# Kernel optimization log

Measured on AMD Instinct MI355X. Metric: run time of the kernel, lower is better.

Reference implementation:

```python
import jax, jax.numpy as jnp
import numpy as np

N = 100000
E = 1250000
D = 64
R = 16


def _glorot(key, shape):
    fan_in, fan_out = shape[-2], shape[-1]
    lim = jnp.sqrt(6.0 / (fan_in + fan_out))
    return jax.random.uniform(key, shape, jnp.float32, -lim, lim)


def setup_inputs() -> dict:
    key = jax.random.key(0)
    ks = jax.random.split(key, 9)
    x = jax.random.normal(ks[0], (N, D), jnp.float32)
    edge_index = jax.random.randint(ks[1], (2, E), 0, N, jnp.int64 if jax.config.jax_enable_x64 else jnp.int32).astype(jnp.int32)
    edge_type = jax.random.randint(ks[2], (E,), 0, R).astype(jnp.int32)
    return {
        "x": x,
        "edge_index": edge_index,
        "edge_type": edge_type,
        "W1": _glorot(ks[3], (R, D, D)),
        "sw1": _glorot(ks[4], (D, D)),
        "b1": jnp.zeros((D,), jnp.float32),
        "W2": _glorot(ks[5], (R, D, D)),
        "sw2": _glorot(ks[6], (D, D)),
        "b2": jnp.zeros((D,), jnp.float32),
    }


def _rgcn_layer(x, src, dst, edge_type, W, sw, b, residual):
    # self transform [N, O]
    out = x @ sw
    # per-relation transform of all nodes: [N, R, O] (avoids [E, D, O] gathered weights,
    # same math as bmm(x_j, W[edge_type]))
    xW = jnp.einsum('nd,rdo->nro', x, W)
    msg = xW[src, edge_type]                      # [E, O] per-edge messages
    agg = jax.ops.segment_sum(msg, dst, num_segments=N)  # scatter-add aggregate
    out = out + agg
    if residual:
        out = out + x  # Identity residual (in == out channels)
    out = out + b
    return jax.nn.relu(out)


def reference(x, edge_index, edge_type, W1, sw1, b1, W2, sw2, b2):
    src, dst = edge_index[0], edge_index[1]
    # layer 1: residual=True; layer 2: encoding=False -> no residual.
    # activation (relu) applied after every layer by RGCN.forward; dropout p=0 / eval -> no-op.
    h = _rgcn_layer(x, src, dst, edge_type, W1, sw1, b1, residual=True)
    h = _rgcn_layer(h, src, dst, edge_type, W2, sw2, b2, residual=False)
    return h
```

## Files before the change

kernel.cpp:

```cpp
#include <hip/hip_runtime.h>
#include <hip/hip_bf16.h>

#define NN 100000
#define NE 1250000
#define DD 64
#define RR 16
#define NP 17
#define NTILE 6250

typedef __attribute__((ext_vector_type(8))) short s16x8;
typedef __attribute__((ext_vector_type(4))) float f32x4;

static __device__ __forceinline__ unsigned short f2bf(float v) {
    __hip_bfloat16 h = __float2bfloat16(v);
    return __builtin_bit_cast(unsigned short, h);
}
static __device__ __forceinline__ float bf2f(unsigned short u) {
    unsigned int w = ((unsigned int)u) << 16;
    return __builtin_bit_cast(float, w);
}
static __device__ __forceinline__ unsigned int pack2(float a, float b) {
    return ((unsigned int)f2bf(b) << 16) | (unsigned int)f2bf(a);
}


__global__ void hist_dst(const int* __restrict__ dst, int* __restrict__ cnt) {
    int e = blockIdx.x * 256 + threadIdx.x;
    if (e < NE) atomicAdd(&cnt[dst[e]], 1);
}

__global__ __launch_bounds__(256) void scan1(const int* __restrict__ cnt,
                                             int* __restrict__ rp, int* __restrict__ part) {
    __shared__ int s[256];
    int i = blockIdx.x * 256 + threadIdx.x;
    int v = (i < NN) ? cnt[i] : 0;
    s[threadIdx.x] = v;
    __syncthreads();
    for (int off = 1; off < 256; off <<= 1) {
        int t = (threadIdx.x >= off) ? s[threadIdx.x - off] : 0;
        __syncthreads();
        s[threadIdx.x] += t;
        __syncthreads();
    }
    if (i < NN) rp[i] = s[threadIdx.x] - v;
    if (threadIdx.x == 255) part[blockIdx.x] = s[255];
}

#define NBLK_SCAN 391
__global__ void scan2(int* __restrict__ part, int* __restrict__ rp) {
    __shared__ int s[NBLK_SCAN];
    if (threadIdx.x < NBLK_SCAN) s[threadIdx.x] = part[threadIdx.x];
    __syncthreads();
    if (threadIdx.x == 0) {
        int acc = 0;
        for (int b = 0; b < NBLK_SCAN; ++b) { int t = s[b]; s[b] = acc; acc += t; }
        rp[NN] = NE;
    }
    __syncthreads();
    if (threadIdx.x < NBLK_SCAN) part[threadIdx.x] = s[threadIdx.x];
}

__global__ void scan3(int* __restrict__ rp, const int* __restrict__ part, int* __restrict__ cur) {
    int i = blockIdx.x * 256 + threadIdx.x;
    if (i < NN) {
        int v = rp[i] + part[blockIdx.x];
        rp[i] = v;
        cur[i] = v;
    }
}

__global__ void scatter_dst(const int* __restrict__ src, const int* __restrict__ dst,
                            const int* __restrict__ et, int* __restrict__ cur,
                            int* __restrict__ sg) {
    int e = blockIdx.x * 256 + threadIdx.x;
    if (e >= NE) return;
    int p = atomicAdd(&cur[dst[e]], 1);
    sg[p] = et[e] * NN + src[e];
}


__global__ void prep_w2(const float* __restrict__ W1, const float* __restrict__ sw1,
                        const float* __restrict__ W2, const float* __restrict__ sw2,
                        unsigned short* __restrict__ wt) {
    int i = blockIdx.x * 256 + threadIdx.x;
    if (i >= 2 * NP * DD * DD) return;
    int d = i & 63;
    int o = (i >> 6) & 63;
    int p = (i >> 12) % NP;
    int l = i / (NP * DD * DD);
    const float* src;
    if (p < 16) src = (l ? W2 : W1) + p * DD * DD;
    else        src = (l ? sw2 : sw1);
    wt[i] = f2bf(src[d * DD + o]);
}

__global__ void prep_x2(const float* __restrict__ x, unsigned short* __restrict__ xb) {
    int i = blockIdx.x * blockDim.x + threadIdx.x;
    if (i < NN * DD) xb[i] = f2bf(x[i]);
}

__global__ __launch_bounds__(256) void xw_kernel(
    const unsigned short* __restrict__ xb,
    const unsigned short* __restrict__ wt,
    unsigned short* __restrict__ tab)
{
    const int wid  = threadIdx.x >> 6;
    const int lane = threadIdx.x & 63;
    const int c = lane & 15;
    const int q = lane >> 4;
    const int t = blockIdx.x * 4 + wid;
    if (t >= NTILE) return;
    const int n0 = t * 16;
    const int p0 = blockIdx.y * 4;
    const int p1 = min(p0 + 4, NP);

    const unsigned short* xrow = xb + (size_t)(n0 + c) * DD + q * 8;
    s16x8 b0 = *(const s16x8*)(xrow);
    s16x8 b1 = *(const s16x8*)(xrow + 32);

    for (int p = p0; p < p1; ++p) {
        const unsigned short* wp = wt + p * (DD * DD);
        uint2* orow = (uint2*)(tab + ((size_t)p * NN + n0 + c) * DD);
        #pragma unroll
        for (int nb = 0; nb < 4; ++nb) {
            const unsigned short* wrow = wp + (nb * 16 + c) * DD + q * 8;
            s16x8 a0 = *(const s16x8*)(wrow);
            s16x8 a1 = *(const s16x8*)(wrow + 32);
            f32x4 acc = {0.f, 0.f, 0.f, 0.f};
            acc = __builtin_amdgcn_mfma_f32_16x16x32_bf16(a0, b0, acc, 0, 0, 0);
            acc = __builtin_amdgcn_mfma_f32_16x16x32_bf16(a1, b1, acc, 0, 0, 0);
            uint2 pk;
            pk.x = pack2(acc[0], acc[1]);
            pk.y = pack2(acc[2], acc[3]);
            orow[nb * 4 + q] = pk;
        }
    }
}

__global__ __launch_bounds__(256) void agg_kernel(
    const unsigned short* __restrict__ tab,
    const int* __restrict__ rp,
    const int* __restrict__ sg,
    const float* __restrict__ bias,
    const float* __restrict__ xres,
    float* __restrict__ outf,
    unsigned short* __restrict__ outb)
{
    const int wid  = threadIdx.x >> 6;
    const int lane = threadIdx.x & 63;
    const int n = blockIdx.x * 4 + wid;
    const int h  = lane >> 5;
    const int ol = lane & 31;

    float a0 = 0.f, a1 = 0.f;
    int e = rp[n];
    const int e1 = rp[n + 1];
    for (; e + 4 <= e1; e += 4) {
        int r0 = sg[e + h];
        int r1 = sg[e + 2 + h];
        unsigned int u0 = *(const unsigned int*)(tab + (size_t)r0 * DD + ol * 2);
        unsigned int u1 = *(const unsigned int*)(tab + (size_t)r1 * DD + ol * 2);
        a0 += bf2f((unsigned short)u0) + bf2f((unsigned short)u1);
        a1 += bf2f((unsigned short)(u0 >> 16)) + bf2f((unsigned short)(u1 >> 16));
    }
    for (; e + 2 <= e1; e += 2) {
        int r0 = sg[e + h];
        unsigned int u0 = *(const unsigned int*)(tab + (size_t)r0 * DD + ol * 2);
        a0 += bf2f((unsigned short)u0);
        a1 += bf2f((unsigned short)(u0 >> 16));
    }
    if (e < e1 && h == 0) {
        int r0 = sg[e];
        unsigned int u0 = *(const unsigned int*)(tab + (size_t)r0 * DD + ol * 2);
        a0 += bf2f((unsigned short)u0);
        a1 += bf2f((unsigned short)(u0 >> 16));
    }
    a0 += __shfl_xor(a0, 32, 64);
    a1 += __shfl_xor(a1, 32, 64);

    {
        unsigned int u = *(const unsigned int*)(tab + ((size_t)16 * NN + n) * DD + ol * 2);
        a0 += bf2f((unsigned short)u);
        a1 += bf2f((unsigned short)(u >> 16));
    }
    const float2 bv = *(const float2*)(bias + ol * 2);
    a0 += bv.x; a1 += bv.y;
    if (xres) {
        const float2 rv = *(const float2*)(xres + (size_t)n * DD + ol * 2);
        a0 += rv.x; a1 += rv.y;
    }
    a0 = fmaxf(a0, 0.f);
    a1 = fmaxf(a1, 0.f);

    if (h == 0) {
        if (outb)
            *(unsigned int*)(outb + (size_t)n * DD + ol * 2) = pack2(a0, a1);
        if (outf) {
            float2 v = {a0, a1};
            *(float2*)(outf + (size_t)n * DD + ol * 2) = v;
        }
    }
}


extern "C" void kernel_launch(void* const* d_in, const int* in_sizes, int n_in,
                              void* d_out, int out_size, void* d_ws, size_t ws_size,
                              hipStream_t stream)
{
    (void)in_sizes; (void)n_in; (void)out_size; (void)ws_size;
    const float* x    = (const float*)d_in[0];
    const int*   ei   = (const int*)d_in[1];
    const int*   et   = (const int*)d_in[2];
    const float* W1   = (const float*)d_in[3];
    const float* sw1  = (const float*)d_in[4];
    const float* b1   = (const float*)d_in[5];
    const float* W2   = (const float*)d_in[6];
    const float* sw2  = (const float*)d_in[7];
    const float* b2   = (const float*)d_in[8];
    float* out = (float*)d_out;

    const int* src = ei;
    const int* dst = ei + NE;

    char* ws = (char*)d_ws;

    unsigned short* tab  = (unsigned short*)(ws);
    unsigned short* xb   = (unsigned short*)(ws + 217600000);
    unsigned short* h1b  = (unsigned short*)(ws + 230400000);
    unsigned short* wt2  = (unsigned short*)(ws + 243200000);
    int* sg   = (int*)(ws + 243478528);
    int* rp   = (int*)(ws + 248478528);
    int* cur  = (int*)(ws + 248878544);
    int* cnt  = (int*)(ws + 249278544);
    int* part = (int*)(ws + 249678544);

    const int NB_E    = (NE + 255) / 256;
    const int NB_ELEM = (NN * DD + 255) / 256;

    hipMemsetAsync(cnt, 0, NN * sizeof(int), stream);
    hist_dst<<<NB_E, 256, 0, stream>>>(dst, cnt);
    scan1<<<NBLK_SCAN, 256, 0, stream>>>(cnt, rp, part);
    scan2<<<1, 512, 0, stream>>>(part, rp);
    scan3<<<NBLK_SCAN, 256, 0, stream>>>(rp, part, cur);
    scatter_dst<<<NB_E, 256, 0, stream>>>(src, dst, et, cur, sg);

    prep_w2<<<(2 * NP * DD * DD + 255) / 256, 256, 0, stream>>>(W1, sw1, W2, sw2, wt2);
    prep_x2<<<NB_ELEM, 256, 0, stream>>>(x, xb);

    const int NB_XW  = (NTILE + 3) / 4;
    const int NB_AGG = NN / 4;

    xw_kernel<<<dim3(NB_XW, 5), 256, 0, stream>>>(xb, wt2, tab);
    agg_kernel<<<NB_AGG, 256, 0, stream>>>(tab, rp, sg, b1, x, nullptr, h1b);

    xw_kernel<<<dim3(NB_XW, 5), 256, 0, stream>>>(h1b, wt2 + NP * DD * DD, tab);
    agg_kernel<<<NB_AGG, 256, 0, stream>>>(tab, rp, sg, b2, nullptr, out, nullptr);
}
```

Before: 598.2 us.

## Split relation table into two halves to shrink gather working set

Edges are now bucketed by destination and relation half (relations 0-7 and 8-15), and each layer computes and aggregates in two phases, each using a 9-slot (or 8-slot) transformed-feature table instead of a 17-slot one. A float carry buffer holds the partial sum between phases. The intent is to halve the footprint of the randomly gathered table so more of it stays in cache. The cost is extra launches, a carry write and read per node, and twice the passes over the CSR offsets.

```diff
diff --git a/kernel.cpp b/kernel.cpp
--- a/kernel.cpp
+++ b/kernel.cpp
@@ -5,8 +5,10 @@
 #define NE 1250000
 #define DD 64
 #define RR 16
-#define NP 17
+#define NSLOT 9
 #define NTILE 6250
+#define NBINS 200000
+#define NBLK2 782
 
 typedef __attribute__((ext_vector_type(8))) short s16x8;
 typedef __attribute__((ext_vector_type(4))) float f32x4;
@@ -24,16 +26,17 @@
 }
 
 
-__global__ void hist_dst(const int* __restrict__ dst, int* __restrict__ cnt) {
+__global__ void hist_key(const int* __restrict__ dst, const int* __restrict__ et,
+                         int* __restrict__ cnt) {
     int e = blockIdx.x * 256 + threadIdx.x;
-    if (e < NE) atomicAdd(&cnt[dst[e]], 1);
+    if (e < NE) atomicAdd(&cnt[dst[e] * 2 + (et[e] >> 3)], 1);
 }
 
 __global__ __launch_bounds__(256) void scan1(const int* __restrict__ cnt,
                                              int* __restrict__ rp, int* __restrict__ part) {
     __shared__ int s[256];
     int i = blockIdx.x * 256 + threadIdx.x;
-    int v = (i < NN) ? cnt[i] : 0;
+    int v = (i < NBINS) ? cnt[i] : 0;
     s[threadIdx.x] = v;
     __syncthreads();
     for (int off = 1; off < 256; off <<= 1) {
@@ -42,40 +45,40 @@
         s[threadIdx.x] += t;
         __syncthreads();
     }
-    if (i < NN) rp[i] = s[threadIdx.x] - v;
+    if (i < NBINS) rp[i] = s[threadIdx.x] - v;
     if (threadIdx.x == 255) part[blockIdx.x] = s[255];
 }
 
-#define NBLK_SCAN 391
-__global__ void scan2(int* __restrict__ part, int* __restrict__ rp) {
-    __shared__ int s[NBLK_SCAN];
-    if (threadIdx.x < NBLK_SCAN) s[threadIdx.x] = part[threadIdx.x];
+__global__ __launch_bounds__(1024) void scan2(int* __restrict__ part, int* __restrict__ rp) {
+    __shared__ int s[NBLK2];
+    if (threadIdx.x < NBLK2) s[threadIdx.x] = part[threadIdx.x];
     __syncthreads();
     if (threadIdx.x == 0) {
         int acc = 0;
-        for (int b = 0; b < NBLK_SCAN; ++b) { int t = s[b]; s[b] = acc; acc += t; }
-        rp[NN] = NE;
+        for (int b = 0; b < NBLK2; ++b) { int t = s[b]; s[b] = acc; acc += t; }
+        rp[NBINS] = NE;
     }
     __syncthreads();
-    if (threadIdx.x < NBLK_SCAN) part[threadIdx.x] = s[threadIdx.x];
+    if (threadIdx.x < NBLK2) part[threadIdx.x] = s[threadIdx.x];
 }
 
 __global__ void scan3(int* __restrict__ rp, const int* __restrict__ part, int* __restrict__ cur) {
     int i = blockIdx.x * 256 + threadIdx.x;
-    if (i < NN) {
+    if (i < NBINS) {
         int v = rp[i] + part[blockIdx.x];
         rp[i] = v;
         cur[i] = v;
     }
 }
 
-__global__ void scatter_dst(const int* __restrict__ src, const int* __restrict__ dst,
+__global__ void scatter_key(const int* __restrict__ src, const int* __restrict__ dst,
                             const int* __restrict__ et, int* __restrict__ cur,
                             int* __restrict__ sg) {
     int e = blockIdx.x * 256 + threadIdx.x;
     if (e >= NE) return;
-    int p = atomicAdd(&cur[dst[e]], 1);
-    sg[p] = et[e] * NN + src[e];
+    int r = et[e];
+    int p = atomicAdd(&cur[dst[e] * 2 + (r >> 3)], 1);
+    sg[p] = (r & 7) * NN + src[e];
 }
 
 
@@ -83,15 +86,18 @@
                         const float* __restrict__ W2, const float* __restrict__ sw2,
                         unsigned short* __restrict__ wt) {
     int i = blockIdx.x * 256 + threadIdx.x;
-    if (i >= 2 * NP * DD * DD) return;
+    if (i >= 2 * 17 * DD * DD) return;
     int d = i & 63;
     int o = (i >> 6) & 63;
-    int p = (i >> 12) % NP;
-    int l = i / (NP * DD * DD);
-    const float* src;
-    if (p < 16) src = (l ? W2 : W1) + p * DD * DD;
-    else        src = (l ? sw2 : sw1);
-    wt[i] = f2bf(src[d * DD + o]);
+    int s = (i >> 12) % 17;
+    int l = i / (17 * DD * DD);
+    const float* W  = l ? W2 : W1;
+    const float* sw = l ? sw2 : sw1;
+    const float* srcp;
+    if (s < 8)       srcp = W + s * DD * DD;
+    else if (s == 8) srcp = sw;
+    else             srcp = W + (s - 1) * DD * DD;
+    wt[i] = f2bf(srcp[d * DD + o]);
 }
 
 __global__ void prep_x2(const float* __restrict__ x, unsigned short* __restrict__ xb) {
@@ -102,7 +108,8 @@
 __global__ __launch_bounds__(256) void xw_kernel(
     const unsigned short* __restrict__ xb,
     const unsigned short* __restrict__ wt,
-    unsigned short* __restrict__ tab)
+    unsigned short* __restrict__ tab,
+    int np)
 {
     const int wid  = threadIdx.x >> 6;
     const int lane = threadIdx.x & 63;
@@ -111,8 +118,8 @@
     const int t = blockIdx.x * 4 + wid;
     if (t >= NTILE) return;
     const int n0 = t * 16;
-    const int p0 = blockIdx.y * 4;
-    const int p1 = min(p0 + 4, NP);
+    const int p0 = blockIdx.y * 3;
+    const int p1 = min(p0 + 3, np);
 
     const unsigned short* xrow = xb + (size_t)(n0 + c) * DD + q * 8;
     s16x8 b0 = *(const s16x8*)(xrow);
@@ -139,12 +146,14 @@
 
 __global__ __launch_bounds__(256) void agg_kernel(
     const unsigned short* __restrict__ tab,
-    const int* __restrict__ rp,
+    const int* __restrict__ rp2,
     const int* __restrict__ sg,
+    int phase,
     const float* __restrict__ bias,
     const float* __restrict__ xres,
-    float* __restrict__ outf,
-    unsigned short* __restrict__ outb)
+    float* __restrict__ carry,
+    unsigned short* __restrict__ outb,
+    float* __restrict__ outf)
 {
     const int wid  = threadIdx.x >> 6;
     const int lane = threadIdx.x & 63;
@@ -153,8 +162,8 @@
     const int ol = lane & 31;
 
     float a0 = 0.f, a1 = 0.f;
-    int e = rp[n];
-    const int e1 = rp[n + 1];
+    int e = rp2[n * 2 + phase];
+    const int e1 = rp2[n * 2 + phase + 1];
     for (; e + 4 <= e1; e += 4) {
         int r0 = sg[e + h];
         int r1 = sg[e + 2 + h];
@@ -178,26 +187,32 @@
     a0 += __shfl_xor(a0, 32, 64);
     a1 += __shfl_xor(a1, 32, 64);
 
-    {
-        unsigned int u = *(const unsigned int*)(tab + ((size_t)16 * NN + n) * DD + ol * 2);
+    if (phase == 0) {
+        unsigned int u = *(const unsigned int*)(tab + ((size_t)8 * NN + n) * DD + ol * 2);
         a0 += bf2f((unsigned short)u);
         a1 += bf2f((unsigned short)(u >> 16));
-    }
-    const float2 bv = *(const float2*)(bias + ol * 2);
-    a0 += bv.x; a1 += bv.y;
-    if (xres) {
-        const float2 rv = *(const float2*)(xres + (size_t)n * DD + ol * 2);
-        a0 += rv.x; a1 += rv.y;
-    }
-    a0 = fmaxf(a0, 0.f);
-    a1 = fmaxf(a1, 0.f);
-
-    if (h == 0) {
-        if (outb)
-            *(unsigned int*)(outb + (size_t)n * DD + ol * 2) = pack2(a0, a1);
-        if (outf) {
+        const float2 bv = *(const float2*)(bias + ol * 2);
+        a0 += bv.x; a1 += bv.y;
+        if (xres) {
+            const float2 rv = *(const float2*)(xres + (size_t)n * DD + ol * 2);
+            a0 += rv.x; a1 += rv.y;
+        }
+        if (h == 0) {
             float2 v = {a0, a1};
-            *(float2*)(outf + (size_t)n * DD + ol * 2) = v;
+            *(float2*)(carry + (size_t)n * DD + ol * 2) = v;
+        }
+    } else {
+        const float2 cv = *(const float2*)(carry + (size_t)n * DD + ol * 2);
+        a0 += cv.x; a1 += cv.y;
+        a0 = fmaxf(a0, 0.f);
+        a1 = fmaxf(a1, 0.f);
+        if (h == 0) {
+            if (outb)
+                *(unsigned int*)(outb + (size_t)n * DD + ol * 2) = pack2(a0, a1);
+            if (outf) {
+                float2 v = {a0, a1};
+                *(float2*)(outf + (size_t)n * DD + ol * 2) = v;
+            }
         }
     }
 }
@@ -224,35 +239,41 @@
 
     char* ws = (char*)d_ws;
 
-    unsigned short* tab  = (unsigned short*)(ws);
-    unsigned short* xb   = (unsigned short*)(ws + 217600000);
-    unsigned short* h1b  = (unsigned short*)(ws + 230400000);
-    unsigned short* wt2  = (unsigned short*)(ws + 243200000);
-    int* sg   = (int*)(ws + 243478528);
-    int* rp   = (int*)(ws + 248478528);
-    int* cur  = (int*)(ws + 248878544);
-    int* cnt  = (int*)(ws + 249278544);
-    int* part = (int*)(ws + 249678544);
+    unsigned short* tab   = (unsigned short*)(ws);
+    unsigned short* xb    = (unsigned short*)(ws + 115200000);
+    unsigned short* h1b   = (unsigned short*)(ws + 128000000);
+    float*          carry = (float*)(ws + 140800000);
+    unsigned short* wt2   = (unsigned short*)(ws + 166400000);
+    int* sg   = (int*)(ws + 166678528);
+    int* rp2  = (int*)(ws + 171678528);
+    int* cur  = (int*)(ws + 172478532);
+    int* cnt  = (int*)(ws + 173278532);
+    int* part = (int*)(ws + 174078532);
 
     const int NB_E    = (NE + 255) / 256;
     const int NB_ELEM = (NN * DD + 255) / 256;
 
-    hipMemsetAsync(cnt, 0, NN * sizeof(int), stream);
-    hist_dst<<<NB_E, 256, 0, stream>>>(dst, cnt);
-    scan1<<<NBLK_SCAN, 256, 0, stream>>>(cnt, rp, part);
-    scan2<<<1, 512, 0, stream>>>(part, rp);
-    scan3<<<NBLK_SCAN, 256, 0, stream>>>(rp, part, cur);
-    scatter_dst<<<NB_E, 256, 0, stream>>>(src, dst, et, cur, sg);
-
-    prep_w2<<<(2 * NP * DD * DD + 255) / 256, 256, 0, stream>>>(W1, sw1, W2, sw2, wt2);
+    hipMemsetAsync(cnt, 0, NBINS * sizeof(int), stream);
+    hist_key<<<NB_E, 256, 0, stream>>>(dst, et, cnt);
+    scan1<<<NBLK2, 256, 0, stream>>>(cnt, rp2, part);
+    scan2<<<1, 1024, 0, stream>>>(part, rp2);
+    scan3<<<NBLK2, 256, 0, stream>>>(rp2, part, cur);
+    scatter_key<<<NB_E, 256, 0, stream>>>(src, dst, et, cur, sg);
+
+    prep_w2<<<(2 * 17 * DD * DD + 255) / 256, 256, 0, stream>>>(W1, sw1, W2, sw2, wt2);
     prep_x2<<<NB_ELEM, 256, 0, stream>>>(x, xb);
 
     const int NB_XW  = (NTILE + 3) / 4;
     const int NB_AGG = NN / 4;
-
-    xw_kernel<<<dim3(NB_XW, 5), 256, 0, stream>>>(xb, wt2, tab);
-    agg_kernel<<<NB_AGG, 256, 0, stream>>>(tab, rp, sg, b1, x, nullptr, h1b);
-
-    xw_kernel<<<dim3(NB_XW, 5), 256, 0, stream>>>(h1b, wt2 + NP * DD * DD, tab);
-    agg_kernel<<<NB_AGG, 256, 0, stream>>>(tab, rp, sg, b2, nullptr, out, nullptr);
-}
+    const int WPL = 17 * DD * DD;
+
+    xw_kernel<<<dim3(NB_XW, 3), 256, 0, stream>>>(xb, wt2, tab, 9);
+    agg_kernel<<<NB_AGG, 256, 0, stream>>>(tab, rp2, sg, 0, b1, x, carry, nullptr, nullptr);
+    xw_kernel<<<dim3(NB_XW, 3), 256, 0, stream>>>(xb, wt2 + 9 * DD * DD, tab, 8);
+    agg_kernel<<<NB_AGG, 256, 0, stream>>>(tab, rp2, sg, 1, nullptr, nullptr, carry, h1b, nullptr);
+
+    xw_kernel<<<dim3(NB_XW, 3), 256, 0, stream>>>(h1b, wt2 + WPL, tab, 9);
+    agg_kernel<<<NB_AGG, 256, 0, stream>>>(tab, rp2, sg, 0, b2, nullptr, carry, nullptr, nullptr);
+    xw_kernel<<<dim3(NB_XW, 3), 256, 0, stream>>>(h1b, wt2 + WPL + 9 * DD * DD, tab, 8);
+    agg_kernel<<<NB_AGG, 256, 0, stream>>>(tab, rp2, sg, 1, nullptr, nullptr, carry, nullptr, out);
+}
```

Measured after the change: 675.6 us. 12.9% more time.

## Compute transforms only for used (relation, source) pairs and aggregate via edge chunks

Applied to the files above, without the earlier changes.

Builds a compacted list of the (relation, source) keys that actually appear in the edge list. The per-relation transform is computed only for those rows instead of for all 16 relations times every node, which shrinks the intermediate table that gets written and read. The self-transform, bias and residual move into separate fp32 kernels that write a carry buffer. Aggregation switches from one wave per destination node to fixed edge chunks, with segmented sums flushed by float atomics, and a finalize kernel applies ReLU. The cost is extra preprocessing passes (flag, scan, remap), more kernel launches, float atomic traffic, and non-deterministic summation order.

```diff
diff --git a/kernel.cpp b/kernel.cpp
--- a/kernel.cpp
+++ b/kernel.cpp
@@ -5,8 +5,10 @@
 #define NE 1250000
 #define DD 64
 #define RR 16
-#define NP 17
-#define NTILE 6250
+#define NKEY 1600000
+#define NTILEC 78125
+#define NBLK_SCAN 391
+#define NBLK_KEY 6250
 
 typedef __attribute__((ext_vector_type(8))) short s16x8;
 typedef __attribute__((ext_vector_type(4))) float f32x4;
@@ -24,6 +26,62 @@
 }
 
 
+__global__ void flag_key(const int* __restrict__ src, const int* __restrict__ et,
+                         unsigned char* __restrict__ flagK) {
+    int e = blockIdx.x * 256 + threadIdx.x;
+    if (e < NE) flagK[et[e] * NN + src[e]] = 1;
+}
+
+__global__ __launch_bounds__(256) void scanA(const unsigned char* __restrict__ flagK,
+                                             int* __restrict__ rowmap, int* __restrict__ partK) {
+    __shared__ int s[256];
+    int i = blockIdx.x * 256 + threadIdx.x;
+    int v = flagK[i] ? 1 : 0;
+    s[threadIdx.x] = v;
+    __syncthreads();
+    for (int off = 1; off < 256; off <<= 1) {
+        int t = (threadIdx.x >= off) ? s[threadIdx.x - off] : 0;
+        __syncthreads();
+        s[threadIdx.x] += t;
+        __syncthreads();
+    }
+    rowmap[i] = s[threadIdx.x] - v;
+    if (threadIdx.x == 255) partK[blockIdx.x] = s[255];
+}
+
+__global__ __launch_bounds__(1024) void scanB(int* __restrict__ partK) {
+    __shared__ int s[1024];
+    int t = threadIdx.x;
+    int b0 = t * 7, b1 = min(b0 + 7, NBLK_KEY);
+    int loc[7];
+    int sum = 0;
+    for (int j = b0; j < b1; ++j) { loc[j - b0] = partK[j]; sum += loc[j - b0]; }
+    s[t] = sum;
+    __syncthreads();
+    for (int off = 1; off < 1024; off <<= 1) {
+        int v = (t >= off) ? s[t - off] : 0;
+        __syncthreads();
+        s[t] += v;
+        __syncthreads();
+    }
+    int excl = s[t] - sum;
+    for (int j = b0; j < b1; ++j) { int v = loc[j - b0]; partK[j] = excl; excl += v; }
+}
+
+__global__ void scanC_emit(const unsigned char* __restrict__ flagK, int* __restrict__ rowmap,
+                           const int* __restrict__ partK,
+                           int* __restrict__ rsrc, int* __restrict__ rrel) {
+    int i = blockIdx.x * 256 + threadIdx.x;
+    int rid = rowmap[i] + partK[blockIdx.x];
+    rowmap[i] = rid;
+    if (flagK[i]) {
+        int rel = i / NN;
+        rsrc[rid] = i - rel * NN;
+        rrel[rid] = rel;
+    }
+}
+
+
 __global__ void hist_dst(const int* __restrict__ dst, int* __restrict__ cnt) {
     int e = blockIdx.x * 256 + threadIdx.x;
     if (e < NE) atomicAdd(&cnt[dst[e]], 1);
@@ -46,15 +104,13 @@
     if (threadIdx.x == 255) part[blockIdx.x] = s[255];
 }
 
-#define NBLK_SCAN 391
-__global__ void scan2(int* __restrict__ part, int* __restrict__ rp) {
+__global__ void scan2(int* __restrict__ part) {
     __shared__ int s[NBLK_SCAN];
     if (threadIdx.x < NBLK_SCAN) s[threadIdx.x] = part[threadIdx.x];
     __syncthreads();
     if (threadIdx.x == 0) {
         int acc = 0;
         for (int b = 0; b < NBLK_SCAN; ++b) { int t = s[b]; s[b] = acc; acc += t; }
-        rp[NN] = NE;
     }
     __syncthreads();
     if (threadIdx.x < NBLK_SCAN) part[threadIdx.x] = s[threadIdx.x];
@@ -69,29 +125,38 @@
     }
 }
 
-__global__ void scatter_dst(const int* __restrict__ src, const int* __restrict__ dst,
-                            const int* __restrict__ et, int* __restrict__ cur,
-                            int* __restrict__ sg) {
+__global__ void scatter2(const int* __restrict__ src, const int* __restrict__ dst,
+                         const int* __restrict__ et, const int* __restrict__ rowmap,
+                         int* __restrict__ cur, int2* __restrict__ sgd) {
     int e = blockIdx.x * 256 + threadIdx.x;
     if (e >= NE) return;
-    int p = atomicAdd(&cur[dst[e]], 1);
-    sg[p] = et[e] * NN + src[e];
-}
-
-
-__global__ void prep_w2(const float* __restrict__ W1, const float* __restrict__ sw1,
-                        const float* __restrict__ W2, const float* __restrict__ sw2,
-                        unsigned short* __restrict__ wt) {
-    int i = blockIdx.x * 256 + threadIdx.x;
-    if (i >= 2 * NP * DD * DD) return;
+    int d = dst[e];
+    int row = rowmap[et[e] * NN + src[e]];
+    int p = atomicAdd(&cur[d], 1);
+    sgd[p] = make_int2(row, d);
+}
+
+
+__global__ void prep_w(const float* __restrict__ W1, const float* __restrict__ W2,
+                       unsigned short* __restrict__ wt) {
+    int i = blockIdx.x * 256 + threadIdx.x;
+    if (i >= 2 * RR * DD * DD) return;
     int d = i & 63;
     int o = (i >> 6) & 63;
-    int p = (i >> 12) % NP;
-    int l = i / (NP * DD * DD);
-    const float* src;
-    if (p < 16) src = (l ? W2 : W1) + p * DD * DD;
-    else        src = (l ? sw2 : sw1);
-    wt[i] = f2bf(src[d * DD + o]);
+    int r = (i >> 12) & 15;
+    int l = i >> 16;
+    const float* W = l ? W2 : W1;
+    wt[i] = f2bf(W[(r * DD + d) * DD + o]);
+}
+
+__global__ void prep_swT(const float* __restrict__ sw1, const float* __restrict__ sw2,
+                         float* __restrict__ swT) {
+    int i = blockIdx.x * 256 + threadIdx.x;
+    if (i >= 2 * DD * DD) return;
+    int d = i & 63;
+    int o = (i >> 6) & 63;
+    int l = i >> 12;
+    swT[i] = (l ? sw2 : sw1)[d * DD + o];
 }
 
 __global__ void prep_x2(const float* __restrict__ x, unsigned short* __restrict__ xb) {
@@ -99,28 +164,37 @@
     if (i < NN * DD) xb[i] = f2bf(x[i]);
 }
 
-__global__ __launch_bounds__(256) void xw_kernel(
+
+__global__ __launch_bounds__(256) void xw_c(
     const unsigned short* __restrict__ xb,
     const unsigned short* __restrict__ wt,
-    unsigned short* __restrict__ tab)
+    const int* __restrict__ rsrc,
+    const int* __restrict__ rrel,
+    unsigned short* __restrict__ tabc)
 {
     const int wid  = threadIdx.x >> 6;
     const int lane = threadIdx.x & 63;
     const int c = lane & 15;
     const int q = lane >> 4;
-    const int t = blockIdx.x * 4 + wid;
-    if (t >= NTILE) return;
-    const int n0 = t * 16;
-    const int p0 = blockIdx.y * 4;
-    const int p1 = min(p0 + 4, NP);
-
-    const unsigned short* xrow = xb + (size_t)(n0 + c) * DD + q * 8;
+    const int tile = blockIdx.x * 4 + wid;
+    if (tile >= NTILEC) return;
+    const int row0 = tile * 16;
+
+    const int myrel = rrel[row0 + c];
+    const int r_lo = __shfl(myrel, 0, 64);
+    if (r_lo > 15) return;
+    const int r_hi = min(__shfl(myrel, 15, 64), 15);
+
+    const int srcn = rsrc[row0 + c];
+    const unsigned short* xrow = xb + (size_t)srcn * DD + q * 8;
     s16x8 b0 = *(const s16x8*)(xrow);
     s16x8 b1 = *(const s16x8*)(xrow + 32);
 
-    for (int p = p0; p < p1; ++p) {
-        const unsigned short* wp = wt + p * (DD * DD);
-        uint2* orow = (uint2*)(tab + ((size_t)p * NN + n0 + c) * DD);
+    uint2* orow = (uint2*)(tabc + (size_t)(row0 + c) * DD);
+
+    for (int r = r_lo; r <= r_hi; ++r) {
+        const unsigned short* wp = wt + r * (DD * DD);
+        const bool mine = (myrel == r);
         #pragma unroll
         for (int nb = 0; nb < 4; ++nb) {
             const unsigned short* wrow = wp + (nb * 16 + c) * DD + q * 8;
@@ -129,77 +203,112 @@
             f32x4 acc = {0.f, 0.f, 0.f, 0.f};
             acc = __builtin_amdgcn_mfma_f32_16x16x32_bf16(a0, b0, acc, 0, 0, 0);
             acc = __builtin_amdgcn_mfma_f32_16x16x32_bf16(a1, b1, acc, 0, 0, 0);
-            uint2 pk;
-            pk.x = pack2(acc[0], acc[1]);
-            pk.y = pack2(acc[2], acc[3]);
-            orow[nb * 4 + q] = pk;
+            if (mine) {
+                uint2 pk;
+                pk.x = pack2(acc[0], acc[1]);
+                pk.y = pack2(acc[2], acc[3]);
+                orow[nb * 4 + q] = pk;
+            }
         }
     }
 }
 
+__global__ __launch_bounds__(256) void self_f32(
+    const float* __restrict__ h, const float* __restrict__ swT,
+    const float* __restrict__ bias, const float* __restrict__ xres,
+    float* __restrict__ carry)
+{
+    int idx = blockIdx.x * 256 + threadIdx.x;
+    if (idx >= NN * DD) return;
+    int o = idx & 63;
+    int n = idx >> 6;
+    const float4* xrow = (const float4*)(h + (size_t)n * DD);
+    const float4* srow = (const float4*)(swT + o * DD);
+    float acc = bias[o];
+    if (xres) acc += xres[idx];
+    #pragma unroll
+    for (int j = 0; j < 16; ++j) {
+        float4 a = xrow[j], w = srow[j];
+        acc += a.x * w.x + a.y * w.y + a.z * w.z + a.w * w.w;
+    }
+    carry[idx] = acc;
+}
+
+__global__ __launch_bounds__(256) void self_bf(
+    const unsigned short* __restrict__ hb, const float* __restrict__ swT,
+    const float* __restrict__ bias, float* __restrict__ carry)
+{
+    int idx = blockIdx.x * 256 + threadIdx.x;
+    if (idx >= NN * DD) return;
+    int o = idx & 63;
+    int n = idx >> 6;
+    const unsigned int* hrow = (const unsigned int*)(hb + (size_t)n * DD);
+    const float2* srow = (const float2*)(swT + o * DD);
+    float acc = bias[o];
+    #pragma unroll
+    for (int j = 0; j < 32; ++j) {
+        unsigned int u = hrow[j];
+        float2 w = srow[j];
+        acc += bf2f((unsigned short)u) * w.x + bf2f((unsigned short)(u >> 16)) * w.y;
+    }
+    carry[idx] = acc;
+}
+
+#define CHUNK 64
 __global__ __launch_bounds__(256) void agg_kernel(
-    const unsigned short* __restrict__ tab,
-    const int* __restrict__ rp,
-    const int* __restrict__ sg,
-    const float* __restrict__ bias,
-    const float* __restrict__ xres,
-    float* __restrict__ outf,
-    unsigned short* __restrict__ outb)
+    const unsigned int* __restrict__ tab32,
+    const int2* __restrict__ sgd,
+    float* __restrict__ carry)
 {
     const int wid  = threadIdx.x >> 6;
     const int lane = threadIdx.x & 63;
-    const int n = blockIdx.x * 4 + wid;
     const int h  = lane >> 5;
     const int ol = lane & 31;
+    const int e0 = (blockIdx.x * 4 + wid) * CHUNK;
+    if (e0 >= NE) return;
 
     float a0 = 0.f, a1 = 0.f;
-    int e = rp[n];
-    const int e1 = rp[n + 1];
-    for (; e + 4 <= e1; e += 4) {
-        int r0 = sg[e + h];
-        int r1 = sg[e + 2 + h];
-        unsigned int u0 = *(const unsigned int*)(tab + (size_t)r0 * DD + ol * 2);
-        unsigned int u1 = *(const unsigned int*)(tab + (size_t)r1 * DD + ol * 2);
-        a0 += bf2f((unsigned short)u0) + bf2f((unsigned short)u1);
-        a1 += bf2f((unsigned short)(u0 >> 16)) + bf2f((unsigned short)(u1 >> 16));
-    }
-    for (; e + 2 <= e1; e += 2) {
-        int r0 = sg[e + h];
-        unsigned int u0 = *(const unsigned int*)(tab + (size_t)r0 * DD + ol * 2);
-        a0 += bf2f((unsigned short)u0);
-        a1 += bf2f((unsigned short)(u0 >> 16));
-    }
-    if (e < e1 && h == 0) {
-        int r0 = sg[e];
-        unsigned int u0 = *(const unsigned int*)(tab + (size_t)r0 * DD + ol * 2);
-        a0 += bf2f((unsigned short)u0);
-        a1 += bf2f((unsigned short)(u0 >> 16));
-    }
-    a0 += __shfl_xor(a0, 32, 64);
-    a1 += __shfl_xor(a1, 32, 64);
-
-    {
-        unsigned int u = *(const unsigned int*)(tab + ((size_t)16 * NN + n) * DD + ol * 2);
-        a0 += bf2f((unsigned short)u);
-        a1 += bf2f((unsigned short)(u >> 16));
-    }
-    const float2 bv = *(const float2*)(bias + ol * 2);
-    a0 += bv.x; a1 += bv.y;
-    if (xres) {
-        const float2 rv = *(const float2*)(xres + (size_t)n * DD + ol * 2);
-        a0 += rv.x; a1 += rv.y;
-    }
-    a0 = fmaxf(a0, 0.f);
-    a1 = fmaxf(a1, 0.f);
-
-    if (h == 0) {
-        if (outb)
-            *(unsigned int*)(outb + (size_t)n * DD + ol * 2) = pack2(a0, a1);
-        if (outf) {
-            float2 v = {a0, a1};
-            *(float2*)(outf + (size_t)n * DD + ol * 2) = v;
+    int cur = -1;
+    for (int base = 0; base < CHUNK; base += 16) {
+        int rowk[8], dk[8];
+        unsigned int uk[8];
+        #pragma unroll
+        for (int j = 0; j < 8; ++j) {
+            int e = e0 + base + 2 * j + h;
+            if (e < NE) { int2 g = sgd[e]; rowk[j] = g.x; dk[j] = g.y; }
+            else dk[j] = -1;
         }
-    }
+        #pragma unroll
+        for (int j = 0; j < 8; ++j)
+            if (dk[j] >= 0) uk[j] = tab32[(size_t)rowk[j] * 32 + ol];
+        #pragma unroll
+        for (int j = 0; j < 8; ++j) {
+            if (dk[j] < 0) continue;
+            if (dk[j] != cur) {
+                if (cur >= 0) {
+                    unsafeAtomicAdd(&carry[(size_t)cur * DD + ol * 2],     a0);
+                    unsafeAtomicAdd(&carry[(size_t)cur * DD + ol * 2 + 1], a1);
+                }
+                a0 = 0.f; a1 = 0.f;
+                cur = dk[j];
+            }
+            a0 += bf2f((unsigned short)uk[j]);
+            a1 += bf2f((unsigned short)(uk[j] >> 16));
+        }
+    }
+    if (cur >= 0) {
+        unsafeAtomicAdd(&carry[(size_t)cur * DD + ol * 2],     a0);
+        unsafeAtomicAdd(&carry[(size_t)cur * DD + ol * 2 + 1], a1);
+    }
+}
+
+__global__ void fin_kernel(const float* __restrict__ carry,
+                           unsigned short* __restrict__ outb, float* __restrict__ outf) {
+    int i = blockIdx.x * 256 + threadIdx.x;
+    if (i >= NN * DD) return;
+    float v = fmaxf(carry[i], 0.f);
+    if (outb) outb[i] = f2bf(v);
+    if (outf) outf[i] = v;
 }
 
 
@@ -219,40 +328,58 @@
     const float* b2   = (const float*)d_in[8];
     float* out = (float*)d_out;
 
-    const int* src = ei;
-    const int* dst = ei + NE;
+    const int* srcA = ei;
+    const int* dstA = ei + NE;
 
     char* ws = (char*)d_ws;
-
-    unsigned short* tab  = (unsigned short*)(ws);
-    unsigned short* xb   = (unsigned short*)(ws + 217600000);
-    unsigned short* h1b  = (unsigned short*)(ws + 230400000);
-    unsigned short* wt2  = (unsigned short*)(ws + 243200000);
-    int* sg   = (int*)(ws + 243478528);
-    int* rp   = (int*)(ws + 248478528);
-    int* cur  = (int*)(ws + 248878544);
-    int* cnt  = (int*)(ws + 249278544);
-    int* part = (int*)(ws + 249678544);
+    unsigned short* tabc  = (unsigned short*)(ws);
+    unsigned short* xb    = (unsigned short*)(ws + 160000000);
+    unsigned short* h1b   = (unsigned short*)(ws + 172800000);
+    float*          carry = (float*)(ws + 185600000);
+    unsigned short* wt2   = (unsigned short*)(ws + 211200000);
+    float*          swT   = (float*)(ws + 211462144);
+    int2*           sgd   = (int2*)(ws + 211494912);
+    int*            rowmap= (int*)(ws + 221494912);
+    unsigned char*  flagK = (unsigned char*)(ws + 227894912);
+    int*            rsrc  = (int*)(ws + 229494912);
+    int*            rrel  = (int*)(ws + 234499008);
+    int*            cnt   = (int*)(ws + 239503104);
+    int*            rp    = (int*)(ws + 239903104);
+    int*            cur   = (int*)(ws + 240303120);
+    int*            partD = (int*)(ws + 240703120);
+    int*            partK = (int*)(ws + 240704720);
 
     const int NB_E    = (NE + 255) / 256;
     const int NB_ELEM = (NN * DD + 255) / 256;
+    const int NB_XWC  = (NTILEC + 3) / 4;
+    const int NB_AGG  = (NE + 4 * CHUNK - 1) / (4 * CHUNK);
+
+    hipMemsetAsync(flagK, 0, 1600000, stream);
+    hipMemsetAsync(rsrc, 0, 5004096, stream);
+    hipMemsetAsync(rrel, 0x3f, 5004096, stream);
+    flag_key<<<NB_E, 256, 0, stream>>>(srcA, et, flagK);
+    scanA<<<NBLK_KEY, 256, 0, stream>>>(flagK, rowmap, partK);
+    scanB<<<1, 1024, 0, stream>>>(partK);
+    scanC_emit<<<NBLK_KEY, 256, 0, stream>>>(flagK, rowmap, partK, rsrc, rrel);
 
     hipMemsetAsync(cnt, 0, NN * sizeof(int), stream);
-    hist_dst<<<NB_E, 256, 0, stream>>>(dst, cnt);
-    scan1<<<NBLK_SCAN, 256, 0, stream>>>(cnt, rp, part);
-    scan2<<<1, 512, 0, stream>>>(part, rp);
-    scan3<<<NBLK_SCAN, 256, 0, stream>>>(rp, part, cur);
-    scatter_dst<<<NB_E, 256, 0, stream>>>(src, dst, et, cur, sg);
-
-    prep_w2<<<(2 * NP * DD * DD + 255) / 256, 256, 0, stream>>>(W1, sw1, W2, sw2, wt2);
+    hist_dst<<<NB_E, 256, 0, stream>>>(dstA, cnt);
+    scan1<<<NBLK_SCAN, 256, 0, stream>>>(cnt, rp, partD);
+    scan2<<<1, 512, 0, stream>>>(partD);
+    scan3<<<NBLK_SCAN, 256, 0, stream>>>(rp, partD, cur);
+    scatter2<<<NB_E, 256, 0, stream>>>(srcA, dstA, et, rowmap, cur, sgd);
+
+    prep_w<<<(2 * RR * DD * DD + 255) / 256, 256, 0, stream>>>(W1, W2, wt2);
+    prep_swT<<<(2 * DD * DD + 255) / 256, 256, 0, stream>>>(sw1, sw2, swT);
     prep_x2<<<NB_ELEM, 256, 0, stream>>>(x, xb);
 
-    const int NB_XW  = (NTILE + 3) / 4;
-    const int NB_AGG = NN / 4;
-
-    xw_kernel<<<dim3(NB_XW, 5), 256, 0, stream>>>(xb, wt2, tab);
-    agg_kernel<<<NB_AGG, 256, 0, stream>>>(tab, rp, sg, b1, x, nullptr, h1b);
-
-    xw_kernel<<<dim3(NB_XW, 5), 256, 0, stream>>>(h1b, wt2 + NP * DD * DD, tab);
-    agg_kernel<<<NB_AGG, 256, 0, stream>>>(tab, rp, sg, b2, nullptr, out, nullptr);
-}
+    self_f32<<<NB_ELEM, 256, 0, stream>>>(x, swT, b1, x, carry);
+    xw_c<<<NB_XWC, 256, 0, stream>>>(xb, wt2, rsrc, rrel, tabc);
+    agg_kernel<<<NB_AGG, 256, 0, stream>>>((const unsigned int*)tabc, sgd, carry);
+    fin_kernel<<<NB_ELEM, 256, 0, stream>>>(carry, h1b, nullptr);
+
+    self_bf<<<NB_ELEM, 256, 0, stream>>>(h1b, swT + DD * DD, b2, carry);
+    xw_c<<<NB_XWC, 256, 0, stream>>>(h1b, wt2 + RR * DD * DD, rsrc, rrel, tabc);
+    agg_kernel<<<NB_AGG, 256, 0, stream>>>((const unsigned int*)tabc, sgd, carry);
+    fin_kernel<<<NB_ELEM, 256, 0, stream>>>(carry, nullptr, out);
+}
```

Measured after the change: 1.137 ms. 1.9x slower.

## Fuse per-relation transform with aggregation via aggregate-then-transform in shared memory

Applied to the files above, without the earlier changes.

Replaces the precompute of a [17,N,64] bf16 table of x·W_r followed by a gather with a single fused kernel per layer. Each block owns 16 destination nodes. It aggregates raw source features per relation into shared-memory fp32 accumulators using LDS atomics, in two passes of 8 relations each, then applies the per-relation weights with MFMA and adds the self transform, bias, residual and ReLU. Edge records are packed into one word holding the source, relation and destination low bits. This removes the large intermediate table write and read, at the cost of LDS atomics, zeroing a large shared buffer, two passes over each block's edges, and a large shared footprint that lowers occupancy.

```diff
diff --git a/kernel.cpp b/kernel.cpp
--- a/kernel.cpp
+++ b/kernel.cpp
@@ -5,8 +5,9 @@
 #define NE 1250000
 #define DD 64
 #define RR 16
-#define NP 17
 #define NTILE 6250
+#define NBLK_SCAN 391
+#define SST 68
 
 typedef __attribute__((ext_vector_type(8))) short s16x8;
 typedef __attribute__((ext_vector_type(4))) float f32x4;
@@ -46,7 +47,6 @@
     if (threadIdx.x == 255) part[blockIdx.x] = s[255];
 }
 
-#define NBLK_SCAN 391
 __global__ void scan2(int* __restrict__ part, int* __restrict__ rp) {
     __shared__ int s[NBLK_SCAN];
     if (threadIdx.x < NBLK_SCAN) s[threadIdx.x] = part[threadIdx.x];
@@ -69,13 +69,15 @@
     }
 }
 
-__global__ void scatter_dst(const int* __restrict__ src, const int* __restrict__ dst,
-                            const int* __restrict__ et, int* __restrict__ cur,
-                            int* __restrict__ sg) {
+__global__ void scatter_pack(const int* __restrict__ src, const int* __restrict__ dst,
+                             const int* __restrict__ et, int* __restrict__ cur,
+                             unsigned int* __restrict__ ep) {
     int e = blockIdx.x * 256 + threadIdx.x;
     if (e >= NE) return;
-    int p = atomicAdd(&cur[dst[e]], 1);
-    sg[p] = et[e] * NN + src[e];
+    int d = dst[e];
+    int p = atomicAdd(&cur[d], 1);
+    ep[p] = (unsigned int)src[e] | ((unsigned int)et[e] << 17)
+          | ((unsigned int)(d & 15) << 21);
 }
 
 
@@ -83,15 +85,15 @@
                         const float* __restrict__ W2, const float* __restrict__ sw2,
                         unsigned short* __restrict__ wt) {
     int i = blockIdx.x * 256 + threadIdx.x;
-    if (i >= 2 * NP * DD * DD) return;
+    if (i >= 2 * 17 * DD * DD) return;
     int d = i & 63;
     int o = (i >> 6) & 63;
-    int p = (i >> 12) % NP;
-    int l = i / (NP * DD * DD);
-    const float* src;
-    if (p < 16) src = (l ? W2 : W1) + p * DD * DD;
-    else        src = (l ? sw2 : sw1);
-    wt[i] = f2bf(src[d * DD + o]);
+    int p = (i >> 12) % 17;
+    int l = i / (17 * DD * DD);
+    const float* srcp;
+    if (p < 16) srcp = (l ? W2 : W1) + p * DD * DD;
+    else        srcp = (l ? sw2 : sw1);
+    wt[i] = f2bf(srcp[d * DD + o]);
 }
 
 __global__ void prep_x2(const float* __restrict__ x, unsigned short* __restrict__ xb) {
@@ -99,106 +101,127 @@
     if (i < NN * DD) xb[i] = f2bf(x[i]);
 }
 
-__global__ __launch_bounds__(256) void xw_kernel(
+__global__ __launch_bounds__(256) void fused_layer(
     const unsigned short* __restrict__ xb,
     const unsigned short* __restrict__ wt,
-    unsigned short* __restrict__ tab)
+    const int* __restrict__ rp,
+    const unsigned int* __restrict__ ep,
+    const float* __restrict__ bias,
+    const float* __restrict__ xres,
+    unsigned short* __restrict__ outb,
+    float* __restrict__ outf)
 {
+    __shared__ float S[8 * 16 * SST];
+    const int n0   = blockIdx.x * 16;
     const int wid  = threadIdx.x >> 6;
     const int lane = threadIdx.x & 63;
     const int c = lane & 15;
     const int q = lane >> 4;
-    const int t = blockIdx.x * 4 + wid;
-    if (t >= NTILE) return;
-    const int n0 = t * 16;
-    const int p0 = blockIdx.y * 4;
-    const int p1 = min(p0 + 4, NP);
-
-    const unsigned short* xrow = xb + (size_t)(n0 + c) * DD + q * 8;
-    s16x8 b0 = *(const s16x8*)(xrow);
-    s16x8 b1 = *(const s16x8*)(xrow + 32);
-
-    for (int p = p0; p < p1; ++p) {
-        const unsigned short* wp = wt + p * (DD * DD);
-        uint2* orow = (uint2*)(tab + ((size_t)p * NN + n0 + c) * DD);
-        #pragma unroll
-        for (int nb = 0; nb < 4; ++nb) {
-            const unsigned short* wrow = wp + (nb * 16 + c) * DD + q * 8;
+    const int h  = lane >> 5;
+    const int ol = lane & 31;
+
+    const int e0 = rp[n0];
+    const int e1 = rp[n0 + 16];
+    const unsigned int* xb32 = (const unsigned int*)xb;
+
+    f32x4 acc = {0.f, 0.f, 0.f, 0.f};
+
+    for (int pass = 0; pass < 2; ++pass) {
+        const int rbase = pass * 8;
+        for (int i = threadIdx.x; i < 8 * 16 * SST; i += 256) S[i] = 0.f;
+        __syncthreads();
+
+        for (int base = e0 + wid * 8; base < e1; base += 32) {
+            unsigned int w[4];
+            int act[4];
+            #pragma unroll
+            for (int j = 0; j < 4; ++j) {
+                int e = base + 2 * j + h;
+                act[j] = (e < e1);
+                w[j] = act[j] ? ep[e] : 0u;
+            }
+            float v0[4], v1[4];
+            #pragma unroll
+            for (int j = 0; j < 4; ++j) {
+                int rel = (w[j] >> 17) & 15;
+                act[j] = act[j] && (rel >= rbase) && (rel < rbase + 8);
+                if (act[j]) {
+                    int srcn = w[j] & 0x1FFFF;
+                    unsigned int u = xb32[(size_t)srcn * 32 + ol];
+                    v0[j] = bf2f((unsigned short)u);
+                    v1[j] = bf2f((unsigned short)(u >> 16));
+                }
+            }
+            #pragma unroll
+            for (int j = 0; j < 4; ++j) {
+                if (act[j]) {
+                    int r8 = ((w[j] >> 17) & 15) - rbase;
+                    int dl = (w[j] >> 21) & 15;
+                    float* sp = &S[(r8 * 16 + dl) * SST + ol * 2];
+                    atomicAdd(sp,     v0[j]);
+                    atomicAdd(sp + 1, v1[j]);
+                }
+            }
+        }
+        __syncthreads();
+
+        for (int rr = 0; rr < 8; ++rr) {
+            const int r = rbase + rr;
+            const float* srow = &S[(rr * 16 + c) * SST + q * 8];
+            const f32x4* s4 = (const f32x4*)srow;
+            f32x4 f0 = s4[0], f1 = s4[1];
+            const f32x4* s4b = (const f32x4*)(srow + 32);
+            f32x4 f2 = s4b[0], f3 = s4b[1];
+            s16x8 b0, b1;
+            #pragma unroll
+            for (int j = 0; j < 4; ++j) {
+                b0[j]     = (short)f2bf(f0[j]);
+                b0[j + 4] = (short)f2bf(f1[j]);
+                b1[j]     = (short)f2bf(f2[j]);
+                b1[j + 4] = (short)f2bf(f3[j]);
+            }
+            const unsigned short* wrow = wt + r * (DD * DD) + (wid * 16 + c) * DD + q * 8;
             s16x8 a0 = *(const s16x8*)(wrow);
             s16x8 a1 = *(const s16x8*)(wrow + 32);
-            f32x4 acc = {0.f, 0.f, 0.f, 0.f};
             acc = __builtin_amdgcn_mfma_f32_16x16x32_bf16(a0, b0, acc, 0, 0, 0);
             acc = __builtin_amdgcn_mfma_f32_16x16x32_bf16(a1, b1, acc, 0, 0, 0);
-            uint2 pk;
-            pk.x = pack2(acc[0], acc[1]);
-            pk.y = pack2(acc[2], acc[3]);
-            orow[nb * 4 + q] = pk;
         }
-    }
-}
-
-__global__ __launch_bounds__(256) void agg_kernel(
-    const unsigned short* __restrict__ tab,
-    const int* __restrict__ rp,
-    const int* __restrict__ sg,
-    const float* __restrict__ bias,
-    const float* __restrict__ xres,
-    float* __restrict__ outf,
-    unsigned short* __restrict__ outb)
-{
-    const int wid  = threadIdx.x >> 6;
-    const int lane = threadIdx.x & 63;
-    const int n = blockIdx.x * 4 + wid;
-    const int h  = lane >> 5;
-    const int ol = lane & 31;
-
-    float a0 = 0.f, a1 = 0.f;
-    int e = rp[n];
-    const int e1 = rp[n + 1];
-    for (; e + 4 <= e1; e += 4) {
-        int r0 = sg[e + h];
-        int r1 = sg[e + 2 + h];
-        unsigned int u0 = *(const unsigned int*)(tab + (size_t)r0 * DD + ol * 2);
-        unsigned int u1 = *(const unsigned int*)(tab + (size_t)r1 * DD + ol * 2);
-        a0 += bf2f((unsigned short)u0) + bf2f((unsigned short)u1);
-        a1 += bf2f((unsigned short)(u0 >> 16)) + bf2f((unsigned short)(u1 >> 16));
-    }
-    for (; e + 2 <= e1; e += 2) {
-        int r0 = sg[e + h];
-        unsigned int u0 = *(const unsigned int*)(tab + (size_t)r0 * DD + ol * 2);
-        a0 += bf2f((unsigned short)u0);
-        a1 += bf2f((unsigned short)(u0 >> 16));
-    }
-    if (e < e1 && h == 0) {
-        int r0 = sg[e];
-        unsigned int u0 = *(const unsigned int*)(tab + (size_t)r0 * DD + ol * 2);
-        a0 += bf2f((unsigned short)u0);
-        a1 += bf2f((unsigned short)(u0 >> 16));
-    }
-    a0 += __shfl_xor(a0, 32, 64);
-    a1 += __shfl_xor(a1, 32, 64);
+        __syncthreads();
+    }
 
     {
-        unsigned int u = *(const unsigned int*)(tab + ((size_t)16 * NN + n) * DD + ol * 2);
-        a0 += bf2f((unsigned short)u);
-        a1 += bf2f((unsigned short)(u >> 16));
-    }
-    const float2 bv = *(const float2*)(bias + ol * 2);
-    a0 += bv.x; a1 += bv.y;
+        const unsigned short* xrow = xb + (size_t)(n0 + c) * DD + q * 8;
+        s16x8 b0 = *(const s16x8*)(xrow);
+        s16x8 b1 = *(const s16x8*)(xrow + 32);
+        const unsigned short* wrow = wt + 16 * (DD * DD) + (wid * 16 + c) * DD + q * 8;
+        s16x8 a0 = *(const s16x8*)(wrow);
+        s16x8 a1 = *(const s16x8*)(wrow + 32);
+        acc = __builtin_amdgcn_mfma_f32_16x16x32_bf16(a0, b0, acc, 0, 0, 0);
+        acc = __builtin_amdgcn_mfma_f32_16x16x32_bf16(a1, b1, acc, 0, 0, 0);
+    }
+
+    const int n = n0 + c;
+    const int obase = wid * 16 + q * 4;
+    const float4 bv = *(const float4*)(bias + obase);
+    acc[0] += bv.x; acc[1] += bv.y; acc[2] += bv.z; acc[3] += bv.w;
     if (xres) {
-        const float2 rv = *(const float2*)(xres + (size_t)n * DD + ol * 2);
-        a0 += rv.x; a1 += rv.y;
-    }
-    a0 = fmaxf(a0, 0.f);
-    a1 = fmaxf(a1, 0.f);
-
-    if (h == 0) {
-        if (outb)
-            *(unsigned int*)(outb + (size_t)n * DD + ol * 2) = pack2(a0, a1);
-        if (outf) {
-            float2 v = {a0, a1};
-            *(float2*)(outf + (size_t)n * DD + ol * 2) = v;
-        }
+        const float4 rv = *(const float4*)(xres + (size_t)n * DD + obase);
+        acc[0] += rv.x; acc[1] += rv.y; acc[2] += rv.z; acc[3] += rv.w;
+    }
+    acc[0] = fmaxf(acc[0], 0.f);
+    acc[1] = fmaxf(acc[1], 0.f);
+    acc[2] = fmaxf(acc[2], 0.f);
+    acc[3] = fmaxf(acc[3], 0.f);
+
+    if (outb) {
+        uint2 pk;
+        pk.x = pack2(acc[0], acc[1]);
+        pk.y = pack2(acc[2], acc[3]);
+        *(uint2*)(outb + (size_t)n * DD + obase) = pk;
+    }
+    if (outf) {
+        float4 v = {acc[0], acc[1], acc[2], acc[3]};
+        *(float4*)(outf + (size_t)n * DD + obase) = v;
     }
 }
 
@@ -219,40 +242,33 @@
     const float* b2   = (const float*)d_in[8];
     float* out = (float*)d_out;
 
-    const int* src = ei;
-    const int* dst = ei + NE;
+    const int* srcA = ei;
+    const int* dstA = ei + NE;
 
     char* ws = (char*)d_ws;
-
-    unsigned short* tab  = (unsigned short*)(ws);
-    unsigned short* xb   = (unsigned short*)(ws + 217600000);
-    unsigned short* h1b  = (unsigned short*)(ws + 230400000);
-    unsigned short* wt2  = (unsigned short*)(ws + 243200000);
-    int* sg   = (int*)(ws + 243478528);
-    int* rp   = (int*)(ws + 248478528);
-    int* cur  = (int*)(ws + 248878544);
-    int* cnt  = (int*)(ws + 249278544);
-    int* part = (int*)(ws + 249678544);
+    unsigned short* xb   = (unsigned short*)(ws);
+    unsigned short* h1b  = (unsigned short*)(ws + 12800000);
+    unsigned short* wt2  = (unsigned short*)(ws + 25600000);
+    unsigned int*   ep   = (unsigned int*)(ws + 25878528);
+    int*            rp   = (int*)(ws + 30878528);
+    int*            cnt  = (int*)(ws + 31278544);
+    int*            cur  = (int*)(ws + 31678544);
+    int*            part = (int*)(ws + 32078544);
 
     const int NB_E    = (NE + 255) / 256;
     const int NB_ELEM = (NN * DD + 255) / 256;
+    const int WPL = 17 * DD * DD;
 
     hipMemsetAsync(cnt, 0, NN * sizeof(int), stream);
-    hist_dst<<<NB_E, 256, 0, stream>>>(dst, cnt);
+    hist_dst<<<NB_E, 256, 0, stream>>>(dstA, cnt);
     scan1<<<NBLK_SCAN, 256, 0, stream>>>(cnt, rp, part);
     scan2<<<1, 512, 0, stream>>>(part, rp);
     scan3<<<NBLK_SCAN, 256, 0, stream>>>(rp, part, cur);
-    scatter_dst<<<NB_E, 256, 0, stream>>>(src, dst, et, cur, sg);
-
-    prep_w2<<<(2 * NP * DD * DD + 255) / 256, 256, 0, stream>>>(W1, sw1, W2, sw2, wt2);
+    scatter_pack<<<NB_E, 256, 0, stream>>>(srcA, dstA, et, cur, ep);
+
+    prep_w2<<<(2 * 17 * DD * DD + 255) / 256, 256, 0, stream>>>(W1, sw1, W2, sw2, wt2);
     prep_x2<<<NB_ELEM, 256, 0, stream>>>(x, xb);
 
-    const int NB_XW  = (NTILE + 3) / 4;
-    const int NB_AGG = NN / 4;
-
-    xw_kernel<<<dim3(NB_XW, 5), 256, 0, stream>>>(xb, wt2, tab);
-    agg_kernel<<<NB_AGG, 256, 0, stream>>>(tab, rp, sg, b1, x, nullptr, h1b);
-
-    xw_kernel<<<dim3(NB_XW, 5), 256, 0, stream>>>(h1b, wt2 + NP * DD * DD, tab);
-    agg_kernel<<<NB_AGG, 256, 0, stream>>>(tab, rp, sg, b2, nullptr, out, nullptr);
-}
+    fused_layer<<<NTILE, 256, 0, stream>>>(xb, wt2, rp, ep, b1, x, h1b, nullptr);
+    fused_layer<<<NTILE, 256, 0, stream>>>(h1b, wt2 + WPL, rp, ep, b2, nullptr, nullptr, out);
+}
```

Measured after the change: 1.194 ms. 2x slower.
